# Kernel tuning notes

Hardware: AMD Instinct MI355X
Metric: run time of the kernel (lower is better)

Reference implementation:

```python
import jax, jax.numpy as jnp
import numpy as np

B = 2
ROW, COL = 63, 84          # resolution
ROW_, COL_ = 32, 42        # resolution_
N = ROW * COL              # 5292 kv tokens
N_ = ROW_ * COL_           # 1344 q tokens
IN_DIM, OUT_DIM = 256, 512
KEY_DIM, NUM_HEADS, ATTN_RATIO, STRIDE = 16, 8, 2, 2
D = ATTN_RATIO * KEY_DIM   # 32 (value dim per head)
DH = D * NUM_HEADS         # 256
NH_KD = KEY_DIM * NUM_HEADS  # 128
H_KV = DH + NH_KD          # 384
SCALE = KEY_DIM ** -0.5
EPS = 1e-5


def _build_bias_idxs():
    # replicates the itertools.product double loop, vectorized; ids ordered by
    # first occurrence in row-major scan (same as dict insertion order).
    r_ = np.arange(ROW_); c_ = np.arange(COL_)
    r = np.arange(ROW); c = np.arange(COL)
    off_r = np.abs(r_[:, None] * STRIDE - r[None, :])      # (32, 63)
    off_c = np.abs(c_[:, None] * STRIDE - c[None, :])      # (42, 84)
    keys = (off_r[:, None, :, None] * 1000 + off_c[None, :, None, :]).reshape(-1)
    _, first_idx, inv = np.unique(keys, return_index=True, return_inverse=True)
    order = np.argsort(first_idx)
    rank = np.empty_like(order); rank[order] = np.arange(len(order))
    idxs = rank[inv].reshape(N_, N).astype(np.int32)
    return idxs, len(order)


def setup_inputs() -> dict:
    key = jax.random.key(0)
    ks = jax.random.split(key, 12)
    idxs_np, n_off = _build_bias_idxs()
    inp = {
        "x": jax.random.normal(ks[0], (B, N, IN_DIM), jnp.float32),
        "kv_w": jax.random.normal(ks[1], (H_KV, IN_DIM), jnp.float32) * (IN_DIM ** -0.5),
        "kv_g": jnp.ones((H_KV,), jnp.float32),
        "kv_b": jnp.zeros((H_KV,), jnp.float32),
        "q_w": jax.random.normal(ks[2], (NH_KD, IN_DIM), jnp.float32) * (IN_DIM ** -0.5),
        "q_g": jnp.ones((NH_KD,), jnp.float32),
        "q_b": jnp.zeros((NH_KD,), jnp.float32),
        "proj_w": jax.random.normal(ks[3], (OUT_DIM, DH), jnp.float32) * (DH ** -0.5),
        "proj_g": jnp.ones((OUT_DIM,), jnp.float32),
        "proj_b": jnp.zeros((OUT_DIM,), jnp.float32),
        "bias_table": jax.random.normal(ks[4], (NUM_HEADS, n_off), jnp.float32) * 0.02,
        "bias_idxs": jnp.asarray(idxs_np),
    }
    return inp


def _linear_bn(x, w, g, b):
    # Linear (no bias) followed by BatchNorm1d in training mode (batch stats
    # over flattened (B*N) dim, biased variance).
    y = jnp.einsum("bnc,oc->bno", x, w)
    flat = y.reshape(-1, y.shape[-1])
    mu = flat.mean(0)
    var = flat.var(0)
    return (y - mu) * (g / jnp.sqrt(var + EPS)) + b


def _hardswish(x):
    return x * jnp.clip(x + 3.0, 0.0, 6.0) / 6.0


def reference(x, kv_w, kv_g, kv_b, q_w, q_g, q_b, proj_w, proj_g, proj_b,
              bias_table, bias_idxs):
    Bx = x.shape[0]
    # kv projection -> split k (KEY_DIM) and v (D) per head
    kv = _linear_bn(x, kv_w, kv_g, kv_b).reshape(Bx, N, NUM_HEADS, KEY_DIM + D)
    k = kv[..., :KEY_DIM].transpose(0, 2, 1, 3)   # (B, H, N, key_dim)
    v = kv[..., KEY_DIM:].transpose(0, 2, 1, 3)   # (B, H, N, d)
    # q: spatial subsample then projection
    xs = x.reshape(Bx, ROW, COL, IN_DIM)[:, ::STRIDE, ::STRIDE].reshape(Bx, N_, IN_DIM)
    q = _linear_bn(xs, q_w, q_g, q_b).reshape(Bx, N_, NUM_HEADS, KEY_DIM).transpose(0, 2, 1, 3)
    # gathered relative position bias: (H, N_, N)
    ab = bias_table[:, bias_idxs]
    attn = jnp.einsum("bhqd,bhkd->bhqk", q, k) * SCALE + ab[None]
    attn = jax.nn.softmax(attn, axis=-1)
    out = jnp.einsum("bhqk,bhkd->bhqd", attn, v)       # (B, H, N_, d)
    out = out.transpose(0, 2, 1, 3).reshape(Bx, N_, DH)
    out = _linear_bn(_hardswish(out), proj_w, proj_g, proj_b)
    return out
```

## Files before the change

### kernel.cpp

```cpp
#include <hip/hip_runtime.h>
#include <hip/hip_bf16.h>
#include <math.h>

#define N_K 5292
#define N_KP 5376
#define N_Q 1344
#define NH_KD 128
#define NROWS 21504
#define LOG2E 1.4426950408889634f
#define MSTAT 16.0f

typedef float f32x4 __attribute__((ext_vector_type(4)));
typedef float f32x2 __attribute__((ext_vector_type(2)));
typedef short short8 __attribute__((ext_vector_type(8)));

__device__ __forceinline__ float fexp2(float x) {
#if __has_builtin(__builtin_amdgcn_exp2f)
    return __builtin_amdgcn_exp2f(x);
#else
    return exp2f(x);
#endif
}

__device__ __forceinline__ unsigned pk_bf16(float a, float b) {
    union { __hip_bfloat162 h; unsigned u; } c;
    c.h = __float22bfloat162_rn(make_float2(a, b));
    return c.u;
}
__device__ __forceinline__ unsigned short f2bf(float a) {
    return (unsigned short)pk_bf16(a, 0.f);
}

__global__ __launch_bounds__(256) void prep_bf16(
    const float* __restrict__ X, const float* __restrict__ kv_w,
    const float* __restrict__ q_w,
    unsigned short* __restrict__ Xb)
{
    int i = blockIdx.x * 256 + threadIdx.x;
    const float* src;
    long off;
    if (i < 677376)       { src = X;      off = i; }
    else if (i < 701952)  { src = kv_w;   off = i - 677376; }
    else if (i < 710144)  { src = q_w;    off = i - 701952; }
    else return;
    float4 v = *(const float4*)(src + off * 4);
    *(uint2*)(Xb + (size_t)i * 4) = make_uint2(pk_bf16(v.x, v.y), pk_bf16(v.z, v.w));
}

__device__ __forceinline__ void gemm_body_bb(
    const unsigned short* __restrict__ A, const unsigned short* __restrict__ W,
    long asrc, int nrow,
    unsigned short (*As)[40], unsigned short (*Bs)[40], f32x4 acc[4])
{
    const int t = threadIdx.x;
    const int w = t >> 6, lane = t & 63, g = lane >> 4, ln = lane & 15;
    const int srow = t >> 2;
    const int sc8 = (t & 3) * 8;

    for (int k0 = 0; k0 < 256; k0 += 32) {
        uint4 a = make_uint4(0, 0, 0, 0);
        if (asrc >= 0) a = *(const uint4*)(A + asrc * 256 + k0 + sc8);
        uint4 b = *(const uint4*)(W + (size_t)nrow * 256 + k0 + sc8);

        __syncthreads();
        *(uint4*)&As[srow][sc8] = a;
        *(uint4*)&Bs[srow][sc8] = b;
        __syncthreads();

        short8 ah = *(const short8*)&As[w * 16 + ln][g * 8];
        #pragma unroll
        for (int nt = 0; nt < 4; ++nt) {
            short8 bh = *(const short8*)&Bs[nt * 16 + ln][g * 8];
            acc[nt] = __builtin_amdgcn_mfma_f32_16x16x32_bf16(ah, bh, acc[nt], 0, 0, 0);
        }
    }
}

__device__ __forceinline__ void gemm_stats(f32x4 acc[4], float* __restrict__ sums,
                                           int n0, int Ncols, float* scratch)
{
    const int t = threadIdx.x;
    const int w = t >> 6, lane = t & 63, g = lane >> 4, ln = lane & 15;
    float s4[4], q4[4];
    #pragma unroll
    for (int nt = 0; nt < 4; ++nt) {
        float s = acc[nt][0] + acc[nt][1] + acc[nt][2] + acc[nt][3];
        float q = fmaf(acc[nt][0], acc[nt][0], fmaf(acc[nt][1], acc[nt][1],
                  fmaf(acc[nt][2], acc[nt][2], acc[nt][3] * acc[nt][3])));
        s += __shfl_xor(s, 16); s += __shfl_xor(s, 32);
        q += __shfl_xor(q, 16); q += __shfl_xor(q, 32);
        s4[nt] = s; q4[nt] = q;
    }
    __syncthreads();
    float* st_s = scratch;
    float* st_q = scratch + 256;
    if (g == 0) {
        #pragma unroll
        for (int nt = 0; nt < 4; ++nt) {
            st_s[(w * 4 + nt) * 16 + ln] = s4[nt];
            st_q[(w * 4 + nt) * 16 + ln] = q4[nt];
        }
    }
    __syncthreads();
    if (t < 64) {
        int nt = t >> 4, c = t & 15;
        float a = 0.f, b2 = 0.f;
        #pragma unroll
        for (int ww = 0; ww < 4; ++ww) {
            a  += st_s[(ww * 4 + nt) * 16 + c];
            b2 += st_q[(ww * 4 + nt) * 16 + c];
        }
        atomicAdd(&sums[n0 + nt * 16 + c], a);
        atomicAdd(&sums[Ncols + n0 + nt * 16 + c], b2);
    }
}

__global__ __launch_bounds__(256) void gemm_qkv(
    const unsigned short* __restrict__ Xb, const unsigned short* __restrict__ kvWb,
    const unsigned short* __restrict__ qWb,
    const float* __restrict__ bias_table, const int* __restrict__ bias_idxs, int n_off,
    unsigned short* __restrict__ Kp, unsigned short* __restrict__ Vpt,
    float* __restrict__ bt_r,
    float* __restrict__ q_y, float* __restrict__ sums_kv, float* __restrict__ sums_q)
{
    __shared__ unsigned short As[64][40], Bs[64][40];
    const int t = threadIdx.x;
    const int w = t >> 6, lane = t & 63, g = lane >> 4, ln = lane & 15;
    const int srow = t >> 2;
    int id = blockIdx.x;

    if (id >= 1104) {
        id -= 1104;
        if (id < 168) {
            int i = id * 256 + t;
            int row = i / 84, j = i - row * 84;
            int slot;
            if (j < 20) {
                int kap = 44 + j;
                slot = 5248 + (((kap & 15) << 2) | (kap >> 4));
            } else {
                slot = 5312 + (j - 20);
            }
            Vpt[(size_t)row * N_KP + slot] = 0;
        } else {
            int i = (id - 168) * 256 + t;
            if (i < 8 * N_K) {
                int h = i / N_K, j = i - h * N_K;
                bt_r[i] = bias_table[h * n_off + bias_idxs[j]] * LOG2E;
            }
        }
        return;
    }

    f32x4 acc[4];
    #pragma unroll
    for (int nt = 0; nt < 4; ++nt) acc[nt] = (f32x4){0.f, 0.f, 0.f, 0.f};

    if (id < 1008) {
        const int xcd = id & 7, id8 = id >> 3;
        const int my = xcd + (id8 / 6) * 8, ny = id8 % 6;
        if (my >= 166) return;
        const int m0 = my * 64, n0 = ny * 64;
        int mrow = m0 + srow;
        long asrc = (mrow < 10584) ? mrow : -1;
        gemm_body_bb(Xb, kvWb, asrc, n0 + srow, As, Bs, acc);

        #pragma unroll
        for (int nt = 0; nt < 4; ++nt) {
            int c = n0 + nt * 16 + ln;
            int hh = c / 48, cc = c - 48 * hh;
            #pragma unroll
            for (int reg = 0; reg < 4; ++reg) {
                int mr = m0 + w * 16 + g * 4 + reg;
                if (mr < 10584) {
                    int bb = mr >= N_K;
                    int key = mr - bb * N_K;
                    unsigned short v16 = f2bf(acc[nt][reg]);
                    if (cc < 16) {
                        Kp[((size_t)(bb * 8 + hh) * N_K + key) * 16 + cc] = v16;
                    } else {
                        int kap = key & 63;
                        int keyp = (key & ~63) | (((kap & 15) << 2) | (kap >> 4));
                        Vpt[((size_t)(bb * 8 + hh) * 32 + cc - 16) * N_KP + keyp] = v16;
                    }
                }
            }
        }
        gemm_stats(acc, sums_kv, n0, 384, (float*)&As[0][0]);
    } else {
        id -= 1008;
        const int xcd = id & 7, id8 = id >> 3;
        const int my = xcd + (id8 / 2) * 8, ny = id8 % 2;
        if (my >= 42) return;
        const int m0 = my * 64, n0 = ny * 64;
        int mrow = m0 + srow;
        int bb = mrow / N_Q;
        int i = mrow - bb * N_Q;
        long asrc = (long)(bb * N_K + (i / 42) * 168 + (i % 42) * 2);
        gemm_body_bb(Xb, qWb, asrc, n0 + srow, As, Bs, acc);

        #pragma unroll
        for (int nt = 0; nt < 4; ++nt)
            #pragma unroll
            for (int reg = 0; reg < 4; ++reg) {
                int mr = m0 + w * 16 + g * 4 + reg;
                q_y[(size_t)mr * 128 + n0 + nt * 16 + ln] = acc[nt][reg];
            }
        gemm_stats(acc, sums_q, n0, 128, (float*)&As[0][0]);
    }
}

__global__ __launch_bounds__(256) void gemm_proj(
    const unsigned short* __restrict__ Ap, const unsigned short* __restrict__ Wp,
    float* __restrict__ Y, float* __restrict__ sums)
{
    __shared__ unsigned short As[64][40], Bs[64][40];
    const int t = threadIdx.x;
    const int w = t >> 6, lane = t & 63, g = lane >> 4, ln = lane & 15;
    const int id = blockIdx.x;
    const int xcd = id & 7, id8 = id >> 3;
    const int my = xcd + (id8 / 8) * 8, ny = id8 % 8;
    if (my >= 42) return;
    const int m0 = my * 64, n0 = ny * 64;

    f32x4 acc[4];
    #pragma unroll
    for (int nt = 0; nt < 4; ++nt) acc[nt] = (f32x4){0.f, 0.f, 0.f, 0.f};
    gemm_body_bb(Ap, Wp, m0 + (t >> 2), n0 + (t >> 2), As, Bs, acc);

    #pragma unroll
    for (int nt = 0; nt < 4; ++nt)
        #pragma unroll
        for (int reg = 0; reg < 4; ++reg) {
            int mr = m0 + w * 16 + g * 4 + reg;
            Y[(size_t)mr * 512 + n0 + nt * 16 + ln] = acc[nt][reg];
        }
    gemm_stats(acc, sums, n0, 512, (float*)&As[0][0]);
}

__global__ __launch_bounds__(256, 5) void attn_mfma(
    const unsigned short* __restrict__ Kp, const unsigned short* __restrict__ Vpt,
    const float* __restrict__ q_y, const float* __restrict__ sums_q,
    const float* __restrict__ q_g, const float* __restrict__ q_b,
    const float* __restrict__ sums_kv, const float* __restrict__ kv_g,
    const float* __restrict__ bt_r,
    float* __restrict__ pl, float* __restrict__ pacc)
{
    const int id = blockIdx.x;
    const int h = id & 7;
    const int z = (id >> 3) & 7;
    const int qt = id >> 6;
    const int b = z >> 2, ks = z & 3;
    const int t = threadIdx.x;
    const int w = t >> 6, lane = t & 63, g = lane >> 4, ln = lane & 15;

    __shared__ unsigned short btm_s[21 * 166];
    __shared__ unsigned short K_s[2][64][24];
    __shared__ unsigned short Vt_s[2][32][72];
    __shared__ unsigned short P_s[4][16][72];

    const int q0 = qt * 64;
    const int kstart = ks * 1344;
    const int kend = (kstart + 1344 < N_K) ? kstart + 1344 : N_K;
    const int ntiles = (kend - kstart + 63) >> 6;
    const bool tail = (ks == 3);

    const int kr0 = kstart / 84;
    const int kr1 = (kend - 1) / 84;
    const int rq2min = (q0 / 42) * 2;
    const int rq2max = ((q0 + 63) / 42) * 2;
    const int dmin_r = rq2min - kr1;
    const int rows = (rq2max - kr0) - dmin_r + 1;
    const int nb = rows * 166;
    const unsigned mxb = (unsigned)((nb - 1) * 2);
    {
        const float* src = bt_r + h * N_K;
        for (int j = t; j < nb; j += 256) {
            int rr = j / 166, ii = j - rr * 166;
            int dr = dmin_r + rr; dr = dr < 0 ? -dr : dr;
            int dc = ii - 83; dc = dc < 0 ? -dc : dc;
            btm_s[j] = f2bf(src[dr * 84 + dc]);
        }
    }

    short8 qfrag = (short8)0;
    if (lane < 32) {
        const float invq = 1.f / 2688.f, invk = 1.f / 10584.f;
        const float post = 0.25f * LOG2E;
        const int c0 = h * 16 + g * 8;
        const int ck = h * 48 + g * 8;
        const float* qp = q_y + (size_t)(b * N_Q + q0 + w * 16 + ln) * NH_KD + c0;
        float vv[8];
        #pragma unroll
        for (int j = 0; j < 8; ++j) {
            float mu  = sums_q[c0 + j] * invq;
            float var = fmaf(-mu, mu, sums_q[128 + c0 + j] * invq);
            float s   = q_g[c0 + j] * rsqrtf(var + 1e-5f) * post;
            float vq  = fmaf(qp[j], s, fmaf(-mu, s, q_b[c0 + j] * post));
            float muk = sums_kv[ck + j] * invk;
            float vrk = fmaf(-muk, muk, sums_kv[384 + ck + j] * invk);
            float sk  = kv_g[ck + j] * rsqrtf(vrk + 1e-5f);
            vv[j] = vq * sk;
        }
        union { short8 s; unsigned u[4]; } qf;
        qf.u[0] = pk_bf16(vv[0], vv[1]); qf.u[1] = pk_bf16(vv[2], vv[3]);
        qf.u[2] = pk_bf16(vv[4], vv[5]); qf.u[3] = pk_bf16(vv[6], vv[7]);
        qfrag = qf.s;
    }

    int baseb[4];
    #pragma unroll
    for (int reg = 0; reg < 4; ++reg) {
        int qg = q0 + w * 16 + g * 4 + reg;
        int rq2 = (qg / 42) * 2;
        int cq2 = (qg % 42) * 2;
        baseb[reg] = ((rq2 - dmin_r) * 166 + cq2 + 83) * 2;
    }
    int offb[4], kcc[4];
    #pragma unroll
    for (int st = 0; st < 4; ++st) {
        int kg = kstart + st * 16 + ln;
        int okr = kg / 84;
        kcc[st] = kg - okr * 84;
        offb[st] = -(okr * 166 + kcc[st]) * 2;
    }

    const unsigned* kp_base = (const unsigned*)Kp + (size_t)(b * 8 + h) * N_K * 8;
    const unsigned short* vp_base = Vpt + (size_t)(b * 8 + h) * 32 * N_KP;
    const int skey = t >> 2, schunk = t & 3;
    const int vrow = t >> 3, vc8 = (t & 7) * 8;

    uint2 kreg; uint4 vreg;
    {
        int kg = kstart + skey; if (kg > N_K - 1) kg = N_K - 1;
        kreg = *(const uint2*)(kp_base + (size_t)kg * 8 + schunk * 2);
        vreg = *(const uint4*)(vp_base + (size_t)vrow * N_KP + kstart + vc8);
    }
    *(uint2*)&K_s[0][skey][schunk * 4] = kreg;
    *(uint4*)&Vt_s[0][vrow][vc8] = vreg;
    __syncthreads();

    f32x2 l2[4];
    #pragma unroll
    for (int reg = 0; reg < 4; ++reg) l2[reg] = (f32x2){0.f, 0.f};
    f32x4 acc0 = {0.f, 0.f, 0.f, 0.f}, acc1 = {0.f, 0.f, 0.f, 0.f};
    const f32x4 minit = {-MSTAT, -MSTAT, -MSTAT, -MSTAT};
    int p = 0;

    for (int it = 0; it < ntiles; ++it) {
        const int k0 = kstart + it * 64;
        const bool notlast = (it + 1 < ntiles);
        if (notlast) {
            int kg = k0 + 64 + skey; if (kg > N_K - 1) kg = N_K - 1;
            kreg = *(const uint2*)(kp_base + (size_t)kg * 8 + schunk * 2);
            vreg = *(const uint4*)(vp_base + (size_t)vrow * N_KP + k0 + 64 + vc8);
        }

        f32x4 sf[4];
        #pragma unroll
        for (int st = 0; st < 4; ++st) {
            short8 bf = (short8)0;
            if (lane < 32) bf = *(const short8*)&K_s[p][st * 16 + ln][g * 8];
            sf[st] = __builtin_amdgcn_mfma_f32_16x16x32_bf16(qfrag, bf, minit, 0, 0, 0);
        }

        float pv[4][4];
        #pragma unroll
        for (int st = 0; st < 4; ++st) {
            #pragma unroll
            for (int reg = 0; reg < 4; ++reg) {
                unsigned ub = (unsigned)(baseb[reg] + offb[st]);
                ub = ub > mxb ? mxb : ub;
                unsigned short bu = *(const unsigned short*)((const char*)btm_s + ub);
                float bias = __uint_as_float(((unsigned)bu) << 16);
                pv[st][reg] = fexp2(sf[st][reg] + bias);
            }
        }
        if (tail && it == ntiles - 1) {
            #pragma unroll
            for (int st = 0; st < 4; ++st) {
                bool bad = (k0 + st * 16 + ln) >= N_K;
                #pragma unroll
                for (int reg = 0; reg < 4; ++reg)
                    pv[st][reg] = bad ? 0.f : pv[st][reg];
            }
        }

        #pragma unroll
        for (int reg = 0; reg < 4; ++reg) {
            l2[reg] += (f32x2){pv[0][reg], pv[2][reg]} + (f32x2){pv[1][reg], pv[3][reg]};
            uint2 pw = make_uint2(pk_bf16(pv[0][reg], pv[1][reg]),
                                  pk_bf16(pv[2][reg], pv[3][reg]));
            *(uint2*)&P_s[w][g * 4 + reg][4 * ln] = pw;
        }
        __asm__ __volatile__("" ::: "memory");

        #pragma unroll
        for (int kt = 0; kt < 2; ++kt) {
            short8 af = *(const short8*)&P_s[w][ln][g * 8 + kt * 32];
            short8 b0 = *(const short8*)&Vt_s[p][ln][g * 8 + kt * 32];
            short8 b1 = *(const short8*)&Vt_s[p][ln + 16][g * 8 + kt * 32];
            acc0 = __builtin_amdgcn_mfma_f32_16x16x32_bf16(af, b0, acc0, 0, 0, 0);
            acc1 = __builtin_amdgcn_mfma_f32_16x16x32_bf16(af, b1, acc1, 0, 0, 0);
        }

        if (notlast) {
            int q2 = p ^ 1;
            *(uint2*)&K_s[q2][skey][schunk * 4] = kreg;
            *(uint4*)&Vt_s[q2][vrow][vc8] = vreg;
            __syncthreads();
            p = q2;
        }

        #pragma unroll
        for (int st = 0; st < 4; ++st) {
            kcc[st] += 64;
            if (kcc[st] >= 84) { kcc[st] -= 84; offb[st] -= 292; }
            else offb[st] -= 128;
        }
    }

    float l[4];
    #pragma unroll
    for (int reg = 0; reg < 4; ++reg) {
        float s = l2[reg][0] + l2[reg][1];
        s += __shfl_xor(s, 1, 16);
        s += __shfl_xor(s, 2, 16);
        s += __shfl_xor(s, 4, 16);
        s += __shfl_xor(s, 8, 16);
        l[reg] = s;
    }

    const int rbase = (b * 8 + h) * N_Q + q0 + w * 16;
    #pragma unroll
    for (int reg = 0; reg < 4; ++reg) {
        int prow = ks * NROWS + rbase + g * 4 + reg;
        pacc[(size_t)prow * 32 + ln]      = acc0[reg];
        pacc[(size_t)prow * 32 + 16 + ln] = acc1[reg];
        if (ln == 0) pl[prow] = l[reg];
    }
}

__global__ __launch_bounds__(256) void combine_kernel(const float* __restrict__ pl,
                                                      const float* __restrict__ pacc,
                                                      const float* __restrict__ sums_kv,
                                                      const float* __restrict__ kv_g,
                                                      const float* __restrict__ kv_b,
                                                      unsigned short* __restrict__ attn_o,
                                                      const float* __restrict__ proj_w,
                                                      unsigned short* __restrict__ projWb)
{
    if (blockIdx.x >= 672) {
        int i = (blockIdx.x - 672) * 256 + threadIdx.x;
        float4 v = *(const float4*)(proj_w + (size_t)i * 4);
        *(uint2*)(projWb + (size_t)i * 4) = make_uint2(pk_bf16(v.x, v.y), pk_bf16(v.z, v.w));
        return;
    }
    int idx = blockIdx.x * 256 + threadIdx.x;
    int r = idx >> 3, e4 = (idx & 7) * 4;
    float L = (pl[r] + pl[NROWS + r]) + (pl[2 * NROWS + r] + pl[3 * NROWS + r]);
    float invL = 1.f / L;
    size_t o = (size_t)r * 32 + e4;
    float4 v0 = *(const float4*)(pacc + o);
    float4 v1 = *(const float4*)(pacc + (size_t)NROWS * 32 + o);
    float4 v2 = *(const float4*)(pacc + (size_t)2 * NROWS * 32 + o);
    float4 v3 = *(const float4*)(pacc + (size_t)3 * NROWS * 32 + o);
    int q = r % N_Q;
    int bh = r / N_Q;
    int hh = bh & 7, b = bh >> 3;
    const int ch = hh * 48 + 16 + e4;
    const float invk = 1.f / 10584.f;
    float hs[4];
    #pragma unroll
    for (int u = 0; u < 4; ++u) {
        float v = (u == 0 ? v0.x + v1.x + v2.x + v3.x :
                   u == 1 ? v0.y + v1.y + v2.y + v3.y :
                   u == 2 ? v0.z + v1.z + v2.z + v3.z :
                            v0.w + v1.w + v2.w + v3.w);
        float mu  = sums_kv[ch + u] * invk;
        float var = fmaf(-mu, mu, sums_kv[384 + ch + u] * invk);
        float s   = kv_g[ch + u] * rsqrtf(var + 1e-5f);
        float tt  = fmaf(-mu, s, kv_b[ch + u]);
        v = fmaf(s, v * invL, tt);
        hs[u] = v * fminf(fmaxf(v + 3.f, 0.f), 6.f) * (1.f / 6.f);
    }
    *(uint2*)(attn_o + (size_t)(b * N_Q + q) * 256 + hh * 32 + e4) =
        make_uint2(pk_bf16(hs[0], hs[1]), pk_bf16(hs[2], hs[3]));
}

__global__ __launch_bounds__(256) void norm_apply(
    const float* __restrict__ Y, const float* __restrict__ sums,
    const float* __restrict__ g, const float* __restrict__ bb,
    float* __restrict__ out, int rows, int cols, float inv_rows)
{
    __shared__ float sc_s[64], sh_s[64];
    const int t = threadIdx.x;
    const int c0 = blockIdx.x * 64;
    if (t < 64) {
        int c = c0 + t;
        float mu  = sums[c] * inv_rows;
        float var = fmaf(-mu, mu, sums[cols + c] * inv_rows);
        float s   = g[c] * rsqrtf(var + 1e-5f);
        sc_s[t] = s;
        sh_s[t] = fmaf(-mu, s, bb[c]);
    }
    __syncthreads();
    const int c4 = (t & 15) * 4;
    float4 scv = *(const float4*)&sc_s[c4];
    float4 shv = *(const float4*)&sh_s[c4];
    for (int r = blockIdx.y * 16 + (t >> 4); r < rows; r += gridDim.y * 16) {
        size_t off = (size_t)r * cols + c0 + c4;
        float4 v = *(const float4*)(Y + off);
        v.x = fmaf(v.x, scv.x, shv.x);
        v.y = fmaf(v.y, scv.y, shv.y);
        v.z = fmaf(v.z, scv.z, shv.z);
        v.w = fmaf(v.w, scv.w, shv.w);
        *(float4*)(out + off) = v;
    }
}

extern "C" void kernel_launch(void* const* d_in, const int* in_sizes, int n_in,
                              void* d_out, int out_size, void* d_ws, size_t ws_size,
                              hipStream_t stream) {
    (void)n_in; (void)out_size; (void)ws_size;
    const float* x      = (const float*)d_in[0];
    const float* kv_w   = (const float*)d_in[1];
    const float* kv_g   = (const float*)d_in[2];
    const float* kv_b   = (const float*)d_in[3];
    const float* q_w    = (const float*)d_in[4];
    const float* q_g    = (const float*)d_in[5];
    const float* q_b    = (const float*)d_in[6];
    const float* proj_w = (const float*)d_in[7];
    const float* proj_g = (const float*)d_in[8];
    const float* proj_b = (const float*)d_in[9];
    const float* bias_table = (const float*)d_in[10];
    const int*   bias_idxs  = (const int*)d_in[11];
    const int    n_off = in_sizes[10] / 8;
    float* out = (float*)d_out;

    float* ws = (float*)d_ws;
    float* q_y  = ws;
    float* pacc = q_y + 2688 * 128;
    float* proj_y = pacc;
    float* pl = pacc + 4 * NROWS * 32;
    unsigned short* attn_o = (unsigned short*)(pl + 4 * NROWS);
    unsigned short* Kp  = attn_o + 2688 * 256;
    unsigned short* Vpt = Kp + 2 * 8 * N_K * 16;
    float* sums_kv = (float*)(Vpt + 2 * 8 * 32 * N_KP);
    float* sums_q  = sums_kv + 768;
    float* sums_p  = sums_q + 256;
    float* bt_r    = sums_p + 1024;

    unsigned short* Xb     = (unsigned short*)pacc;
    unsigned short* kvWb   = Xb + 10584 * 256;
    unsigned short* qWb    = kvWb + 384 * 256;
    unsigned short* projWb = (unsigned short*)q_y;

    hipMemsetAsync(sums_kv, 0, 2048 * sizeof(float), stream);
    prep_bf16<<<2774, 256, 0, stream>>>(x, kv_w, q_w, Xb);
    gemm_qkv<<<1104 + 168 + 166, 256, 0, stream>>>(Xb, kvWb, qWb, bias_table, bias_idxs,
                                                   n_off, Kp, Vpt, bt_r,
                                                   q_y, sums_kv, sums_q);
    attn_mfma<<<1344, 256, 0, stream>>>(Kp, Vpt, q_y, sums_q, q_g, q_b,
                                        sums_kv, kv_g, bt_r, pl, pacc);
    combine_kernel<<<672 + 128, 256, 0, stream>>>(pl, pacc, sums_kv, kv_g, kv_b, attn_o,
                                                  proj_w, projWb);
    gemm_proj<<<384, 256, 0, stream>>>(attn_o, projWb, proj_y, sums_p);
    norm_apply<<<dim3(8, 84), 256, 0, stream>>>(proj_y, sums_p, proj_g, proj_b, out,
                                                2688, 512, 1.f / 2688.f);
}
```

Measured before the change: 191.7 us.

## Fold stats zeroing into prep, prefetch GEMM loads, compute softmax denominator via MFMA

The separate memset of the stats buffers goes away: an extra block in the bf16 prep kernel zeroes them, which removes one launch. The QKV GEMM body now loads the next k-chunk from global memory while the current one is being consumed, and the k loop is fully unrolled. In attention, the row-sum of exp values is accumulated with an extra MFMA against a ones vector instead of VALU adds plus shuffle reductions, and the bias-index clamp is applied only on the tail tile. The row sum now uses bf16-rounded P values, which slightly changes numerics, and the unclamped bias index relies on in-range indices for non-tail tiles.

```diff
diff --git a/kernel.cpp b/kernel.cpp
--- a/kernel.cpp
+++ b/kernel.cpp
@@ -11,7 +11,6 @@
 #define MSTAT 16.0f
 
 typedef float f32x4 __attribute__((ext_vector_type(4)));
-typedef float f32x2 __attribute__((ext_vector_type(2)));
 typedef short short8 __attribute__((ext_vector_type(8)));
 
 __device__ __forceinline__ float fexp2(float x) {
@@ -34,15 +33,21 @@
 __global__ __launch_bounds__(256) void prep_bf16(
     const float* __restrict__ X, const float* __restrict__ kv_w,
     const float* __restrict__ q_w,
-    unsigned short* __restrict__ Xb)
+    unsigned short* __restrict__ Xb, float* __restrict__ sums)
 {
     int i = blockIdx.x * 256 + threadIdx.x;
+    if (i >= 710144) {
+        int j = i - 710144;
+        float4 z = make_float4(0.f, 0.f, 0.f, 0.f);
+        *(float4*)(sums + (size_t)j * 8)     = z;
+        *(float4*)(sums + (size_t)j * 8 + 4) = z;
+        return;
+    }
     const float* src;
     long off;
     if (i < 677376)       { src = X;      off = i; }
     else if (i < 701952)  { src = kv_w;   off = i - 677376; }
-    else if (i < 710144)  { src = q_w;    off = i - 701952; }
-    else return;
+    else                  { src = q_w;    off = i - 701952; }
     float4 v = *(const float4*)(src + off * 4);
     *(uint2*)(Xb + (size_t)i * 4) = make_uint2(pk_bf16(v.x, v.y), pk_bf16(v.z, v.w));
 }
@@ -57,15 +62,21 @@
     const int srow = t >> 2;
     const int sc8 = (t & 3) * 8;
 
+    uint4 a = make_uint4(0, 0, 0, 0);
+    if (asrc >= 0) a = *(const uint4*)(A + asrc * 256 + sc8);
+    uint4 b = *(const uint4*)(W + (size_t)nrow * 256 + sc8);
+
+    #pragma unroll
     for (int k0 = 0; k0 < 256; k0 += 32) {
-        uint4 a = make_uint4(0, 0, 0, 0);
-        if (asrc >= 0) a = *(const uint4*)(A + asrc * 256 + k0 + sc8);
-        uint4 b = *(const uint4*)(W + (size_t)nrow * 256 + k0 + sc8);
-
         __syncthreads();
         *(uint4*)&As[srow][sc8] = a;
         *(uint4*)&Bs[srow][sc8] = b;
         __syncthreads();
+
+        if (k0 < 224) {
+            if (asrc >= 0) a = *(const uint4*)(A + asrc * 256 + k0 + 32 + sc8);
+            b = *(const uint4*)(W + (size_t)nrow * 256 + k0 + 32 + sc8);
+        }
 
         short8 ah = *(const short8*)&As[w * 16 + ln][g * 8];
         #pragma unroll
@@ -308,6 +319,11 @@
         qfrag = qf.s;
     }
 
+    union { short8 s; unsigned u[4]; } onef;
+    #pragma unroll
+    for (int j = 0; j < 4; ++j) onef.u[j] = 0x3F803F80u;
+    const short8 ones = onef.s;
+
     int baseb[4];
     #pragma unroll
     for (int reg = 0; reg < 4; ++reg) {
@@ -326,24 +342,23 @@
     }
 
     const unsigned* kp_base = (const unsigned*)Kp + (size_t)(b * 8 + h) * N_K * 8;
-    const unsigned short* vp_base = Vpt + (size_t)(b * 8 + h) * 32 * N_KP;
     const int skey = t >> 2, schunk = t & 3;
     const int vrow = t >> 3, vc8 = (t & 7) * 8;
+    const unsigned short* vptr = Vpt + (size_t)(b * 8 + h) * 32 * N_KP
+                                     + (size_t)vrow * N_KP + kstart + vc8;
 
     uint2 kreg; uint4 vreg;
     {
         int kg = kstart + skey; if (kg > N_K - 1) kg = N_K - 1;
         kreg = *(const uint2*)(kp_base + (size_t)kg * 8 + schunk * 2);
-        vreg = *(const uint4*)(vp_base + (size_t)vrow * N_KP + kstart + vc8);
+        vreg = *(const uint4*)vptr;
     }
     *(uint2*)&K_s[0][skey][schunk * 4] = kreg;
     *(uint4*)&Vt_s[0][vrow][vc8] = vreg;
     __syncthreads();
 
-    f32x2 l2[4];
-    #pragma unroll
-    for (int reg = 0; reg < 4; ++reg) l2[reg] = (f32x2){0.f, 0.f};
     f32x4 acc0 = {0.f, 0.f, 0.f, 0.f}, acc1 = {0.f, 0.f, 0.f, 0.f};
+    f32x4 accL = {0.f, 0.f, 0.f, 0.f};
     const f32x4 minit = {-MSTAT, -MSTAT, -MSTAT, -MSTAT};
     int p = 0;
 
@@ -353,7 +368,7 @@
         if (notlast) {
             int kg = k0 + 64 + skey; if (kg > N_K - 1) kg = N_K - 1;
             kreg = *(const uint2*)(kp_base + (size_t)kg * 8 + schunk * 2);
-            vreg = *(const uint4*)(vp_base + (size_t)vrow * N_KP + k0 + 64 + vc8);
+            vreg = *(const uint4*)(vptr + 64);
         }
 
         f32x4 sf[4];
@@ -365,30 +380,35 @@
         }
 
         float pv[4][4];
-        #pragma unroll
-        for (int st = 0; st < 4; ++st) {
+        const bool clampit = tail && (it == ntiles - 1);
+        if (!clampit) {
             #pragma unroll
-            for (int reg = 0; reg < 4; ++reg) {
-                unsigned ub = (unsigned)(baseb[reg] + offb[st]);
-                ub = ub > mxb ? mxb : ub;
-                unsigned short bu = *(const unsigned short*)((const char*)btm_s + ub);
-                float bias = __uint_as_float(((unsigned)bu) << 16);
-                pv[st][reg] = fexp2(sf[st][reg] + bias);
+            for (int st = 0; st < 4; ++st) {
+                #pragma unroll
+                for (int reg = 0; reg < 4; ++reg) {
+                    unsigned ub = (unsigned)(baseb[reg] + offb[st]);
+                    unsigned short bu = *(const unsigned short*)((const char*)btm_s + ub);
+                    float bias = __uint_as_float(((unsigned)bu) << 16);
+                    pv[st][reg] = fexp2(sf[st][reg] + bias);
+                }
             }
-        }
-        if (tail && it == ntiles - 1) {
+        } else {
             #pragma unroll
             for (int st = 0; st < 4; ++st) {
                 bool bad = (k0 + st * 16 + ln) >= N_K;
                 #pragma unroll
-                for (int reg = 0; reg < 4; ++reg)
-                    pv[st][reg] = bad ? 0.f : pv[st][reg];
+                for (int reg = 0; reg < 4; ++reg) {
+                    unsigned ub = (unsigned)(baseb[reg] + offb[st]);
+                    ub = ub > mxb ? mxb : ub;
+                    unsigned short bu = *(const unsigned short*)((const char*)btm_s + ub);
+                    float bias = __uint_as_float(((unsigned)bu) << 16);
+                    pv[st][reg] = bad ? 0.f : fexp2(sf[st][reg] + bias);
+                }
             }
         }
 
         #pragma unroll
         for (int reg = 0; reg < 4; ++reg) {
-            l2[reg] += (f32x2){pv[0][reg], pv[2][reg]} + (f32x2){pv[1][reg], pv[3][reg]};
             uint2 pw = make_uint2(pk_bf16(pv[0][reg], pv[1][reg]),
                                   pk_bf16(pv[2][reg], pv[3][reg]));
             *(uint2*)&P_s[w][g * 4 + reg][4 * ln] = pw;
@@ -402,6 +422,7 @@
             short8 b1 = *(const short8*)&Vt_s[p][ln + 16][g * 8 + kt * 32];
             acc0 = __builtin_amdgcn_mfma_f32_16x16x32_bf16(af, b0, acc0, 0, 0, 0);
             acc1 = __builtin_amdgcn_mfma_f32_16x16x32_bf16(af, b1, acc1, 0, 0, 0);
+            accL = __builtin_amdgcn_mfma_f32_16x16x32_bf16(af, ones, accL, 0, 0, 0);
         }
 
         if (notlast) {
@@ -410,6 +431,7 @@
             *(uint4*)&Vt_s[q2][vrow][vc8] = vreg;
             __syncthreads();
             p = q2;
+            vptr += 64;
         }
 
         #pragma unroll
@@ -420,24 +442,13 @@
         }
     }
 
-    float l[4];
-    #pragma unroll
-    for (int reg = 0; reg < 4; ++reg) {
-        float s = l2[reg][0] + l2[reg][1];
-        s += __shfl_xor(s, 1, 16);
-        s += __shfl_xor(s, 2, 16);
-        s += __shfl_xor(s, 4, 16);
-        s += __shfl_xor(s, 8, 16);
-        l[reg] = s;
-    }
-
     const int rbase = (b * 8 + h) * N_Q + q0 + w * 16;
     #pragma unroll
     for (int reg = 0; reg < 4; ++reg) {
         int prow = ks * NROWS + rbase + g * 4 + reg;
         pacc[(size_t)prow * 32 + ln]      = acc0[reg];
         pacc[(size_t)prow * 32 + 16 + ln] = acc1[reg];
-        if (ln == 0) pl[prow] = l[reg];
+        if (ln == 0) pl[prow] = accL[reg];
     }
 }
 
@@ -556,8 +567,7 @@
     unsigned short* qWb    = kvWb + 384 * 256;
     unsigned short* projWb = (unsigned short*)q_y;
 
-    hipMemsetAsync(sums_kv, 0, 2048 * sizeof(float), stream);
-    prep_bf16<<<2774, 256, 0, stream>>>(x, kv_w, q_w, Xb);
+    prep_bf16<<<2775, 256, 0, stream>>>(x, kv_w, q_w, Xb, sums_kv);
     gemm_qkv<<<1104 + 168 + 166, 256, 0, stream>>>(Xb, kvWb, qWb, bias_table, bias_idxs,
                                                    n_off, Kp, Vpt, bt_r,
                                                    q_y, sums_kv, sums_q);
```

Result: no change. 188.3 us (-1.8%).
